# Kernel tuning notes

Measured on AMD Instinct MI355X. Metric: run time of the kernel, lower is better.

Reference implementation:

```python
import jax, jax.numpy as jnp
import numpy as np

GAMMA = 0.5  # triplet_loss_gamma from __init__


def setup_inputs() -> dict:
    key = jax.random.key(0)
    k1, k2, k3 = jax.random.split(key, 3)
    b, n, m = 16, 2048, 2048
    scores = jax.random.normal(k1, (b, n + 1, m + 1), dtype=jnp.float32)
    gt_matches0 = jax.random.randint(k2, (b, n), 0, m, dtype=jnp.int32)
    gt_matches1 = jax.random.randint(k3, (b, m), 0, n, dtype=jnp.int32)
    return {"gt_matches0": gt_matches0, "gt_matches1": gt_matches1, "scores": scores}


def reference(gt_matches0, gt_matches1, scores):
    b, n = gt_matches0.shape
    m = gt_matches1.shape[1]
    # -1 means "unmatched" -> dustbin index (m for rows, n for cols)
    gt0 = jnp.where(gt_matches0 == -1, m, gt_matches0)
    gt1 = jnp.where(gt_matches1 == -1, n, gt_matches1)
    gamma_pos = jnp.maximum(jnp.float32(GAMMA), 0.0)  # clamp value at the matched slot

    # ---- anchor = rows (points in cloud 0) ----
    s0 = scores[:, :n, :]                                   # (b, n, m+1)
    pos0 = jnp.take_along_axis(s0, gt0[:, :, None], axis=2)  # (b, n, 1)
    # original computes -log(exp(pos)) - (-log(exp(neg))) + gamma == neg - pos + gamma
    gap0 = jnp.maximum(s0 - pos0 + GAMMA, 0.0)              # (b, n, m+1)
    # torch version excludes the matched column; its contribution is clamp(gamma, 0)
    sum0 = jnp.sum(gap0, axis=2) - gamma_pos                # (b, n)
    loss_mean = jnp.mean(2.0 * jnp.log(sum0 + 1.0), axis=1)  # (b,)

    # ---- anchor = columns (points in cloud 1) ----
    s1 = scores[:, :, :m]                                   # (b, n+1, m)
    pos1 = jnp.take_along_axis(s1, gt1[:, None, :], axis=1)  # (b, 1, m)
    gap1 = jnp.maximum(s1 - pos1 + GAMMA, 0.0)              # (b, n+1, m)
    sum1 = jnp.sum(gap1, axis=1) - gamma_pos                # (b, m)
    loss_mean2 = jnp.mean(2.0 * jnp.log(sum1 + 1.0), axis=1)  # (b,)

    return (loss_mean + loss_mean2) / 2.0
```

## Files before the change

kernel.cpp:

```cpp
#include <hip/hip_runtime.h>
#include <math.h>

#define BATCH 16
#define NN 2048
#define MM 2048
#define WW 2049
#define GAMMA 0.5f

__global__ __launch_bounds__(256) void gather_kernel(
    const float* __restrict__ scores, const int* __restrict__ gt0,
    const int* __restrict__ gt1, float* __restrict__ q0, float* __restrict__ q1)
{
    int id = blockIdx.x * 256 + threadIdx.x;
    const int half = BATCH * NN;
    if (id < half) {
        int b = id >> 11, i = id & (NN - 1);
        int g = gt0[id];
        g = (g == -1) ? MM : g;
        g = min(max(g, 0), MM);
        q0[id] = scores[(size_t)b * WW * WW + (size_t)i * WW + g] - GAMMA;
    } else {
        int id2 = id - half;
        int b = id2 >> 11, j = id2 & (MM - 1);
        int g = gt1[id2];
        g = (g == -1) ? NN : g;
        g = min(max(g, 0), NN);
        q1[id2] = scores[(size_t)b * WW * WW + (size_t)g * WW + j] - GAMMA;
    }
}

__global__ __launch_bounds__(256) void main_kernel(
    const float* __restrict__ scores, const float* __restrict__ q0,
    const float* __restrict__ q1, float* __restrict__ colsum,
    float* __restrict__ rowacc)
{
    const int b = blockIdx.y;
    const int row0 = blockIdx.x * 32;
    const int nrows = (blockIdx.x == 63) ? 33 : 32;
    const int tid = threadIdx.x;
    const int wave = tid >> 6;
    const int lane = tid & 63;

    const float* sb = scores + (size_t)b * WW * WW;
    const float* q1b = q1 + b * MM;

    float q1v[32];
    float colacc[32];
#pragma unroll
    for (int k = 0; k < 32; ++k) {
        q1v[k] = q1b[lane + 64 * k];
        colacc[k] = 0.0f;
    }

    float rowterm = 0.0f;
    for (int r = wave; r < nrows; r += 4) {
        const int i = row0 + r;
        const bool has_row = (i < NN);
        const float q0i = has_row ? q0[b * NN + i] : 0.0f;
        const float* rowp = sb + (size_t)i * WW;

        float rp = 0.0f;
#pragma unroll
        for (int k = 0; k < 32; ++k) {
            const float s = rowp[lane + 64 * k];
            rp += fmaxf(s, q0i);
            colacc[k] = fmaxf(s, q1v[k]) + colacc[k];
        }
        if (has_row) {
            if (lane == 0)
                rp += fmaxf(rowp[2048], q0i);
#pragma unroll
            for (int off = 32; off; off >>= 1)
                rp += __shfl_xor(rp, off);
            if (lane == 0)
                rowterm += 2.0f * logf(rp - 2049.0f * q0i + 0.5f);
        }
    }
    if (lane == 0)
        unsafeAtomicAdd(&rowacc[b], rowterm);

    __shared__ float cl[4][MM];
#pragma unroll
    for (int k = 0; k < 32; ++k)
        cl[wave][lane + 64 * k] = colacc[k];
    __syncthreads();
    for (int j = tid; j < MM; j += 256) {
        const float v = cl[0][j] + cl[1][j] + cl[2][j] + cl[3][j];
        unsafeAtomicAdd(&colsum[b * MM + j], v);
    }
}

__global__ __launch_bounds__(256) void finalize_kernel(
    const float* __restrict__ colsum, const float* __restrict__ q1,
    const float* __restrict__ rowacc, float* __restrict__ out)
{
    const int b = blockIdx.x;
    const int tid = threadIdx.x;
    const int wave = tid >> 6;
    const int lane = tid & 63;

    float acc = 0.0f;
    for (int j = tid; j < MM; j += 256) {
        const float cs = colsum[b * MM + j] - 2049.0f * q1[b * MM + j];
        acc += 2.0f * logf(cs + 0.5f);
    }

#pragma unroll
    for (int off = 32; off; off >>= 1)
        acc += __shfl_xor(acc, off);

    __shared__ float red[4];
    if (lane == 0) red[wave] = acc;
    __syncthreads();
    if (tid == 0) {
        const float colterms = red[0] + red[1] + red[2] + red[3];
        out[b] = 0.5f * (rowacc[b] * (1.0f / NN) + colterms * (1.0f / MM));
    }
}

extern "C" void kernel_launch(void* const* d_in, const int* in_sizes, int n_in,
                              void* d_out, int out_size, void* d_ws, size_t ws_size,
                              hipStream_t stream) {
    const int* gt0 = (const int*)d_in[0];
    const int* gt1 = (const int*)d_in[1];
    const float* scores = (const float*)d_in[2];
    float* out = (float*)d_out;

    float* ws = (float*)d_ws;
    float* q0     = ws;
    float* q1     = ws + (size_t)BATCH * NN;
    float* colsum = ws + (size_t)2 * BATCH * NN;
    float* rowacc = ws + (size_t)3 * BATCH * NN;

    hipMemsetAsync(colsum, 0, ((size_t)BATCH * MM + BATCH) * sizeof(float), stream);

    gather_kernel<<<(2 * BATCH * NN) / 256, 256, 0, stream>>>(scores, gt0, gt1, q0, q1);

    dim3 grid(64, BATCH);
    main_kernel<<<grid, 256, 0, stream>>>(scores, q0, q1, colsum, rowacc);

    finalize_kernel<<<BATCH, 256, 0, stream>>>(colsum, q1, rowacc, out);
}
```

Measured before the change: 392.1 us.

## Replace atomic column accumulation with per-block partials and two-stage reduction

```diff
diff --git a/kernel.cpp b/kernel.cpp
--- a/kernel.cpp
+++ b/kernel.cpp
@@ -6,6 +6,8 @@
 #define MM 2048
 #define WW 2049
 #define GAMMA 0.5f
+#define NBX 64
+
 
 __global__ __launch_bounds__(256) void gather_kernel(
     const float* __restrict__ scores, const int* __restrict__ gt0,
@@ -31,8 +33,8 @@
 
 __global__ __launch_bounds__(256) void main_kernel(
     const float* __restrict__ scores, const float* __restrict__ q0,
-    const float* __restrict__ q1, float* __restrict__ colsum,
-    float* __restrict__ rowacc)
+    const float* __restrict__ q1, float* __restrict__ colpart,
+    float* __restrict__ rowpart)
 {
     const int b = blockIdx.y;
     const int row0 = blockIdx.x * 32;
@@ -76,46 +78,70 @@
                 rowterm += 2.0f * logf(rp - 2049.0f * q0i + 0.5f);
         }
     }
-    if (lane == 0)
-        unsafeAtomicAdd(&rowacc[b], rowterm);
 
     __shared__ float cl[4][MM];
+    __shared__ float rw[4];
 #pragma unroll
     for (int k = 0; k < 32; ++k)
         cl[wave][lane + 64 * k] = colacc[k];
+    if (lane == 0) rw[wave] = rowterm;
     __syncthreads();
-    for (int j = tid; j < MM; j += 256) {
-        const float v = cl[0][j] + cl[1][j] + cl[2][j] + cl[3][j];
-        unsafeAtomicAdd(&colsum[b * MM + j], v);
-    }
+
+    float* dst = colpart + ((size_t)blockIdx.x * BATCH + b) * MM;
+    for (int j = tid; j < MM; j += 256)
+        dst[j] = cl[0][j] + cl[1][j] + cl[2][j] + cl[3][j];
+    if (tid == 0)
+        rowpart[blockIdx.x * BATCH + b] = rw[0] + rw[1] + rw[2] + rw[3];
 }
 
-__global__ __launch_bounds__(256) void finalize_kernel(
-    const float* __restrict__ colsum, const float* __restrict__ q1,
-    const float* __restrict__ rowacc, float* __restrict__ out)
+__global__ __launch_bounds__(256) void reduce_cols_kernel(
+    const float* __restrict__ colpart, const float* __restrict__ q1,
+    float* __restrict__ colterm)
 {
-    const int b = blockIdx.x;
+    const int b = blockIdx.y;
+    const int j = blockIdx.x * 256 + threadIdx.x;
     const int tid = threadIdx.x;
     const int wave = tid >> 6;
     const int lane = tid & 63;
 
-    float acc = 0.0f;
-    for (int j = tid; j < MM; j += 256) {
-        const float cs = colsum[b * MM + j] - 2049.0f * q1[b * MM + j];
-        acc += 2.0f * logf(cs + 0.5f);
+    float s0 = 0.0f, s1 = 0.0f, s2 = 0.0f, s3 = 0.0f;
+#pragma unroll
+    for (int bx = 0; bx < NBX; bx += 4) {
+        s0 += colpart[((size_t)(bx + 0) * BATCH + b) * MM + j];
+        s1 += colpart[((size_t)(bx + 1) * BATCH + b) * MM + j];
+        s2 += colpart[((size_t)(bx + 2) * BATCH + b) * MM + j];
+        s3 += colpart[((size_t)(bx + 3) * BATCH + b) * MM + j];
     }
+    const float cs = (s0 + s1) + (s2 + s3);
+    float term = 2.0f * logf(cs - 2049.0f * q1[b * MM + j] + 0.5f);
 
 #pragma unroll
     for (int off = 32; off; off >>= 1)
-        acc += __shfl_xor(acc, off);
+        term += __shfl_xor(term, off);
 
     __shared__ float red[4];
-    if (lane == 0) red[wave] = acc;
+    if (lane == 0) red[wave] = term;
     __syncthreads();
-    if (tid == 0) {
-        const float colterms = red[0] + red[1] + red[2] + red[3];
-        out[b] = 0.5f * (rowacc[b] * (1.0f / NN) + colterms * (1.0f / MM));
+    if (tid == 0)
+        colterm[b * 8 + blockIdx.x] = red[0] + red[1] + red[2] + red[3];
+}
+
+__global__ __launch_bounds__(64) void final_kernel(
+    const float* __restrict__ rowpart, const float* __restrict__ colterm,
+    float* __restrict__ out)
+{
+    const int b = blockIdx.x;
+    const int lane = threadIdx.x;
+
+    float rs = rowpart[lane * BATCH + b];
+    float cs = (lane < 8) ? colterm[b * 8 + lane] : 0.0f;
+#pragma unroll
+    for (int off = 32; off; off >>= 1) {
+        rs += __shfl_xor(rs, off);
+        cs += __shfl_xor(cs, off);
     }
+    if (lane == 0)
+        out[b] = 0.5f * (rs * (1.0f / NN) + cs * (1.0f / MM));
 }
 
 extern "C" void kernel_launch(void* const* d_in, const int* in_sizes, int n_in,
@@ -127,17 +153,19 @@
     float* out = (float*)d_out;
 
     float* ws = (float*)d_ws;
-    float* q0     = ws;
-    float* q1     = ws + (size_t)BATCH * NN;
-    float* colsum = ws + (size_t)2 * BATCH * NN;
-    float* rowacc = ws + (size_t)3 * BATCH * NN;
-
-    hipMemsetAsync(colsum, 0, ((size_t)BATCH * MM + BATCH) * sizeof(float), stream);
+    float* q0      = ws;
+    float* q1      = q0 + (size_t)BATCH * NN;
+    float* colpart = q1 + (size_t)BATCH * MM;
+    float* rowpart = colpart + (size_t)NBX * BATCH * MM;
+    float* colterm = rowpart + (size_t)NBX * BATCH;
 
     gather_kernel<<<(2 * BATCH * NN) / 256, 256, 0, stream>>>(scores, gt0, gt1, q0, q1);
 
-    dim3 grid(64, BATCH);
-    main_kernel<<<grid, 256, 0, stream>>>(scores, q0, q1, colsum, rowacc);
+    dim3 grid(NBX, BATCH);
+    main_kernel<<<grid, 256, 0, stream>>>(scores, q0, q1, colpart, rowpart);
 
-    finalize_kernel<<<BATCH, 256, 0, stream>>>(colsum, q1, rowacc, out);
+    dim3 rgrid(8, BATCH);
+    reduce_cols_kernel<<<rgrid, 256, 0, stream>>>(colpart, q1, colterm);
+
+    final_kernel<<<BATCH, 64, 0, stream>>>(rowpart, colterm, out);
 }
```

Result: no change. 386.7 us (-1.4%).
